# Kernel tuning notes

Measured on AMD Instinct MI355X. Metric: run time of the kernel, lower is better.

The kernel has to match this reference:

```python
import jax, jax.numpy as jnp
import numpy as np
import math

B, L, H, D = 4, 2048, 8, 64
FACTOR = 5
SAMPLE_K = min(FACTOR * int(np.ceil(np.log(L))), L)  # U_part = 40
N_TOP = min(FACTOR * int(np.ceil(np.log(L))), L)     # u = 40


def setup_inputs() -> dict:
    key = jax.random.key(0)
    kq, kk, kv, ki = jax.random.split(key, 4)
    queries = jax.random.normal(kq, (B, L, H, D), dtype=jnp.float32)
    keys = jax.random.normal(kk, (B, L, H, D), dtype=jnp.float32)
    values = jax.random.normal(kv, (B, L, H, D), dtype=jnp.float32)
    # ProbSparse random key sampling indices (torch.randint(L_K, (L_Q, sample_k)))
    index_sample = jax.random.randint(ki, (L, SAMPLE_K), 0, L, dtype=jnp.int64)
    return {"queries": queries, "keys": keys, "values": values,
            "index_sample": index_sample}


def reference(queries, keys, values, index_sample):
    # [B, L, H, D] -> [B, H, L, D]
    Q = jnp.transpose(queries, (0, 2, 1, 3))
    K = jnp.transpose(keys, (0, 2, 1, 3))
    V = jnp.transpose(values, (0, 2, 1, 3))
    L_K = K.shape[2]

    # --- _prob_QK ---
    # gather sampled keys per query: [B, H, L_Q, sample_k, D]
    K_sample = K[:, :, index_sample, :]
    # sampled QK dots: [B, H, L_Q, sample_k]
    Q_K_sample = jnp.einsum('bhld,bhlsd->bhls', Q, K_sample)
    # sparsity measurement M = max - mean
    M = Q_K_sample.max(axis=-1) - Q_K_sample.sum(axis=-1) / L_K  # [B, H, L_Q]
    _, M_top = jax.lax.top_k(M, N_TOP)  # [B, H, n_top]
    # gather top queries: [B, H, n_top, D]
    Q_reduce = jnp.take_along_axis(Q, M_top[..., None], axis=2)
    # reduced scores against all keys: [B, H, n_top, L_K]
    scores_top = jnp.einsum('bhud,bhkd->bhuk', Q_reduce, K)

    # --- forward tail ---
    scale = 1.0 / math.sqrt(D)
    attn = jax.nn.softmax(scores_top * scale, axis=-1)  # dropout = identity (eval)
    context = jnp.einsum('bhuk,bhkd->bhud', attn, V)  # [B, H, n_top, D]
    # [B, n_top, H, D]
    return jnp.transpose(context, (0, 2, 1, 3))
```

## Files before the change

### kernel.cpp

```cpp
#include <hip/hip_runtime.h>
#include <hip/hip_bf16.h>

#define BB 4
#define LL 2048
#define HH 8
#define DD 64
#define SK 40
#define NT 40
#define CH 256
#define NCH (LL / CH)
#define QH 20

#define NPH 5
#define PH 8
#define RS 516
#define PBUF (PH * RS)

typedef __attribute__((address_space(1))) const void* gl_ptr_t;
typedef __attribute__((address_space(3))) void*       lds_ptr_t;

__global__ __launch_bounds__(256) void compute_m_kernel(
        const float* __restrict__ Q, const float* __restrict__ K,
        const int* __restrict__ idx, float* __restrict__ M) {
    __shared__ float kbuf[2 * PBUF];
    __shared__ int sidx[SK];

    int blk = blockIdx.x;
    int x = blk & 7, g = blk >> 3;
    int b = x >> 1;
    int l = (g << 1) | (x & 1);
    int t = threadIdx.x;

    if (t < SK) sidx[t] = idx[(size_t)l * SK + t];

    int q  = t & 3;
    int h  = t >> 5;
    int s0 = (t >> 2) & 7;

    const float4* Qb = (const float4*)(Q + ((size_t)b * LL + l) * 512 + h * 64 + q * 16);
    float4 qf0 = Qb[0], qf1 = Qb[1], qf2 = Qb[2], qf3 = Qb[3];

    const float* Kb = K + (size_t)b * LL * 512;

    int wv   = t >> 6;
    int lane = t & 63;
    __syncthreads();

    #define STAGE(p, buf) do {                                                  \
        _Pragma("unroll")                                                       \
        for (int i = 0; i < 4; ++i) {                                           \
            int r  = wv * 2 + (i >> 1);                                         \
            int hf = i & 1;                                                     \
            const float* gsrc = Kb + (size_t)sidx[(p) * PH + r] * 512           \
                              + hf * 256 + lane * 4;                            \
            float* ldst = kbuf + (buf) * PBUF + r * RS + hf * 256;              \
            __builtin_amdgcn_global_load_lds((gl_ptr_t)gsrc, (lds_ptr_t)ldst,   \
                                             16, 0, 0);                         \
        }                                                                       \
    } while (0)

    STAGE(0, 0);
    __syncthreads();

    float mx = -INFINITY, sm = 0.0f;
    #pragma unroll
    for (int p = 0; p < NPH; ++p) {
        if (p < NPH - 1) STAGE(p + 1, (p + 1) & 1);
        const float* kb = kbuf + (p & 1) * PBUF + s0 * RS + h * 64 + q * 16;
        float4 k0 = *(const float4*)(kb);
        float4 k1 = *(const float4*)(kb + 4);
        float4 k2 = *(const float4*)(kb + 8);
        float4 k3 = *(const float4*)(kb + 12);
        float pd = qf0.x * k0.x + qf0.y * k0.y + qf0.z * k0.z + qf0.w * k0.w
                 + qf1.x * k1.x + qf1.y * k1.y + qf1.z * k1.z + qf1.w * k1.w
                 + qf2.x * k2.x + qf2.y * k2.y + qf2.z * k2.z + qf2.w * k2.w
                 + qf3.x * k3.x + qf3.y * k3.y + qf3.z * k3.z + qf3.w * k3.w;
        pd += __shfl_xor(pd, 1, 64);
        pd += __shfl_xor(pd, 2, 64);
        mx = fmaxf(mx, pd);
        sm += pd;
        if (p < NPH - 1) __syncthreads();
    }
    #undef STAGE

    #pragma unroll
    for (int off = 16; off >= 1; off >>= 1) {
        mx = fmaxf(mx, __shfl_xor(mx, off, 64));
        sm += __shfl_xor(sm, off, 64);
    }
    if ((t & 31) == 0)
        M[((size_t)b * HH + h) * LL + l] = mx - sm * (1.0f / (4.0f * (float)LL));
}

__global__ __launch_bounds__(256) void topk_kernel(const float* __restrict__ M,
                                                   int* __restrict__ topi) {
    __shared__ unsigned long long keys[LL];
    __shared__ unsigned long long wmax[4];
    __shared__ int win;
    int bh = blockIdx.x;
    int t  = threadIdx.x;
    int lane = t & 63, w = t >> 6;

    unsigned long long kmax = 0ULL;
    #pragma unroll
    for (int j = 0; j < 8; ++j) {
        int i = t + 256 * j;
        unsigned int bits = __float_as_uint(M[(size_t)bh * LL + i]);
        bits = (bits & 0x80000000u) ? ~bits : (bits | 0x80000000u);
        unsigned long long k = ((unsigned long long)bits << 11)
                             | (unsigned int)(LL - 1 - i);
        keys[i] = k;
        if (k > kmax) kmax = k;
    }
    __syncthreads();

    for (int u = 0; u < NT; ++u) {
        unsigned long long k = kmax;
        #pragma unroll
        for (int off = 32; off >= 1; off >>= 1) {
            unsigned long long o = __shfl_xor(k, off, 64);
            if (o > k) k = o;
        }
        if (lane == 0) wmax[w] = k;
        __syncthreads();
        if (t == 0) {
            unsigned long long k0 = wmax[0];
            if (wmax[1] > k0) k0 = wmax[1];
            if (wmax[2] > k0) k0 = wmax[2];
            if (wmax[3] > k0) k0 = wmax[3];
            int i = (LL - 1) - (int)(k0 & 0x7FF);
            topi[bh * NT + u] = i;
            keys[i] = 0ULL;
            win = i;
        }
        __syncthreads();
        if ((win & 255) == t) {
            kmax = 0ULL;
            #pragma unroll
            for (int j = 0; j < 8; ++j) {
                unsigned long long kk = keys[t + 256 * j];
                if (kk > kmax) kmax = kk;
            }
        }
    }
}

__global__ __launch_bounds__(256, 3) void attn_kernel(
        const float* __restrict__ Q, const float* __restrict__ K,
        const float* __restrict__ V, const int* __restrict__ topi,
        float2* __restrict__ pml, float* __restrict__ po) {
    __shared__ float  qs[QH][DD];
    __shared__ float4 e4buf[4][64];
    __shared__ float  oarea[4][QH][DD];
    __shared__ float  mlarea[4][QH][2];

    int blk = blockIdx.x;
    int qh  = blk >> 8;
    int cc2 = blk & 255;
    int c   = cc2 & (NCH - 1);
    int bh  = cc2 >> 3;
    int h = bh & (HH - 1), b = bh >> 3;
    int t = threadIdx.x, lane = t & 63, w = t >> 6;
    int u0 = qh * QH;

    for (int i = t; i < QH * DD; i += 256) {
        int u = i >> 6, d = i & 63;
        int lq = topi[bh * NT + u0 + u];
        qs[u][d] = Q[(((size_t)b * LL + lq) * HH + h) * DD + d];
    }

    int key = c * CH + w * 64 + lane;
    const float4* kr = (const float4*)&K[(((size_t)b * LL + key) * HH + h) * DD];
    float4 kreg[16];
    #pragma unroll
    for (int j = 0; j < 16; ++j) kreg[j] = kr[j];

    float vcol[64];
    const float* vb = &V[(((size_t)b * LL + c * CH + w * 64) * HH + h) * DD + lane];
    #pragma unroll
    for (int j = 0; j < 64; ++j) vcol[j] = vb[(size_t)j * HH * DD];

    __syncthreads();

    for (int uq = 0; uq < QH / 4; ++uq) {
        float o0 = 0, o1 = 0, o2 = 0, o3 = 0;
        float mv0, mv1, mv2, mv3, lv0, lv1, lv2, lv3;
        float4 ev;
        #pragma unroll
        for (int j = 0; j < 4; ++j) {
            int u = uq * 4 + j;
            const float4* q4 = (const float4*)&qs[u][0];
            float s = 0.0f;
            #pragma unroll
            for (int cc = 0; cc < 16; ++cc) {
                float4 qv = q4[cc];
                s += qv.x * kreg[cc].x + qv.y * kreg[cc].y
                   + qv.z * kreg[cc].z + qv.w * kreg[cc].w;
            }
            s *= 0.125f;
            float m = s;
            #pragma unroll
            for (int off = 32; off >= 1; off >>= 1)
                m = fmaxf(m, __shfl_xor(m, off, 64));
            float e = __expf(s - m);
            float ls = e;
            #pragma unroll
            for (int off = 32; off >= 1; off >>= 1)
                ls += __shfl_xor(ls, off, 64);
            if (j == 0) { mv0 = m; lv0 = ls; ev.x = e; }
            if (j == 1) { mv1 = m; lv1 = ls; ev.y = e; }
            if (j == 2) { mv2 = m; lv2 = ls; ev.z = e; }
            if (j == 3) { mv3 = m; lv3 = ls; ev.w = e; }
        }
        e4buf[w][lane] = ev;
        asm volatile("s_waitcnt lgkmcnt(0)" ::: "memory");
        #pragma unroll
        for (int l2 = 0; l2 < 64; ++l2) {
            float4 e = e4buf[w][l2];
            float  v = vcol[l2];
            o0 += e.x * v; o1 += e.y * v; o2 += e.z * v; o3 += e.w * v;
        }
        oarea[w][uq * 4 + 0][lane] = o0;
        oarea[w][uq * 4 + 1][lane] = o1;
        oarea[w][uq * 4 + 2][lane] = o2;
        oarea[w][uq * 4 + 3][lane] = o3;
        if (lane == 0) {
            mlarea[w][uq * 4 + 0][0] = mv0; mlarea[w][uq * 4 + 0][1] = lv0;
            mlarea[w][uq * 4 + 1][0] = mv1; mlarea[w][uq * 4 + 1][1] = lv1;
            mlarea[w][uq * 4 + 2][0] = mv2; mlarea[w][uq * 4 + 2][1] = lv2;
            mlarea[w][uq * 4 + 3][0] = mv3; mlarea[w][uq * 4 + 3][1] = lv3;
        }
    }
    __syncthreads();

    for (int i = t; i < QH * DD; i += 256) {
        int u = i >> 6, d = i & 63;
        float m0 = mlarea[0][u][0], m1 = mlarea[1][u][0];
        float m2 = mlarea[2][u][0], m3 = mlarea[3][u][0];
        float mb = fmaxf(fmaxf(m0, m1), fmaxf(m2, m3));
        float s0 = __expf(m0 - mb), s1 = __expf(m1 - mb);
        float s2 = __expf(m2 - mb), s3 = __expf(m3 - mb);
        float ob = oarea[0][u][d] * s0 + oarea[1][u][d] * s1
                 + oarea[2][u][d] * s2 + oarea[3][u][d] * s3;
        int gu = u0 + u;
        po[((size_t)(bh * NT + gu) * NCH + c) * DD + d] = ob;
        if (d == 0) {
            float lb = mlarea[0][u][1] * s0 + mlarea[1][u][1] * s1
                     + mlarea[2][u][1] * s2 + mlarea[3][u][1] * s3;
            pml[(bh * NT + gu) * NCH + c] = make_float2(mb, lb);
        }
    }
}

__global__ __launch_bounds__(256) void merge_kernel(
        const float2* __restrict__ pml, const float* __restrict__ po,
        float* __restrict__ out) {
    int wid  = blockIdx.x * 4 + (threadIdx.x >> 6);
    int lane = threadIdx.x & 63;
    int u  = wid % NT;
    int bh = wid / NT;
    int h = bh & (HH - 1), b = bh >> 3;
    int base = (bh * NT + u) * NCH;

    float m = -INFINITY;
    #pragma unroll
    for (int cc = 0; cc < NCH; ++cc) m = fmaxf(m, pml[base + cc].x);
    float lsum = 0.0f, o = 0.0f;
    #pragma unroll
    for (int cc = 0; cc < NCH; ++cc) {
        float2 ml = pml[base + cc];
        float sc = __expf(ml.x - m);
        lsum += ml.y * sc;
        o    += po[(size_t)(base + cc) * DD + lane] * sc;
    }
    out[(((size_t)b * NT + u) * HH + h) * DD + lane] = o / lsum;
}

extern "C" void kernel_launch(void* const* d_in, const int* in_sizes, int n_in,
                              void* d_out, int out_size, void* d_ws, size_t ws_size,
                              hipStream_t stream) {
    const float* Q   = (const float*)d_in[0];
    const float* K   = (const float*)d_in[1];
    const float* V   = (const float*)d_in[2];
    const int*   idx = (const int*)d_in[3];
    float* out = (float*)d_out;

    char* ws = (char*)d_ws;
    float*  M    = (float*)ws;                        ws += (size_t)BB * HH * LL * sizeof(float);
    int*    topi = (int*)ws;                          ws += (size_t)BB * HH * NT * sizeof(int);
    float2* pml  = (float2*)ws;                       ws += (size_t)BB * HH * NT * NCH * sizeof(float2);
    float*  po   = (float*)ws;

    hipLaunchKernelGGL(compute_m_kernel, dim3(BB * LL), dim3(256), 0, stream,
                       Q, K, idx, M);
    hipLaunchKernelGGL(topk_kernel, dim3(BB * HH), dim3(256), 0, stream, M, topi);
    hipLaunchKernelGGL(attn_kernel, dim3(2 * BB * HH * NCH), dim3(256), 0, stream,
                       Q, K, V, topi, pml, po);
    hipLaunchKernelGGL(merge_kernel, dim3(BB * HH * NT / 4), dim3(256), 0, stream,
                       pml, po, out);
}
```

Baseline: 177.4 us.

## Give each wave private K-sample buffers and drop block barriers in compute_m

The sampled-QK kernel now splits the 40 sampled keys into four slices of ten, one per wave. Each wave loads its keys through registers into its own double-buffered LDS slot, replacing the block-wide async global_load_lds staging and the per-phase __syncthreads with a wave-local lgkmcnt wait. The per-wave max and sum partials are combined through a small shared array, with a single barrier at the end. This removes block-level synchronisation from the loop, at the cost of register-staged copies and a final cross-wave reduction.

```diff
diff --git a/kernel.cpp b/kernel.cpp
--- a/kernel.cpp
+++ b/kernel.cpp
@@ -11,19 +11,15 @@
 #define NCH (LL / CH)
 #define QH 20
 
-#define NPH 5
-#define PH 8
+#define WS 10
 #define RS 516
-#define PBUF (PH * RS)
-
-typedef __attribute__((address_space(1))) const void* gl_ptr_t;
-typedef __attribute__((address_space(3))) void*       lds_ptr_t;
 
 __global__ __launch_bounds__(256) void compute_m_kernel(
         const float* __restrict__ Q, const float* __restrict__ K,
         const int* __restrict__ idx, float* __restrict__ M) {
-    __shared__ float kbuf[2 * PBUF];
+    __shared__ float kbuf[4][2][2 * RS];
     __shared__ int sidx[SK];
+    __shared__ float2 mlpart[4][HH];
 
     int blk = blockIdx.x;
     int x = blk & 7, g = blk >> 3;
@@ -33,40 +29,46 @@
 
     if (t < SK) sidx[t] = idx[(size_t)l * SK + t];
 
-    int q  = t & 3;
-    int h  = t >> 5;
-    int s0 = (t >> 2) & 7;
+    int lane = t & 63, w = t >> 6;
+    int s_lo = lane >> 5;
+    int h    = (lane >> 2) & 7;
+    int q    = lane & 3;
 
     const float4* Qb = (const float4*)(Q + ((size_t)b * LL + l) * 512 + h * 64 + q * 16);
     float4 qf0 = Qb[0], qf1 = Qb[1], qf2 = Qb[2], qf3 = Qb[3];
 
     const float* Kb = K + (size_t)b * LL * 512;
 
-    int wv   = t >> 6;
-    int lane = t & 63;
-    __syncthreads();
-
-    #define STAGE(p, buf) do {                                                  \
-        _Pragma("unroll")                                                       \
-        for (int i = 0; i < 4; ++i) {                                           \
-            int r  = wv * 2 + (i >> 1);                                         \
-            int hf = i & 1;                                                     \
-            const float* gsrc = Kb + (size_t)sidx[(p) * PH + r] * 512           \
-                              + hf * 256 + lane * 4;                            \
-            float* ldst = kbuf + (buf) * PBUF + r * RS + hf * 256;              \
-            __builtin_amdgcn_global_load_lds((gl_ptr_t)gsrc, (lds_ptr_t)ldst,   \
-                                             16, 0, 0);                         \
-        }                                                                       \
+    int r  = lane >> 5;
+    int cw = lane & 31;
+    __syncthreads();
+
+    float4 g0, g1, g2, g3;
+    #define LOADP(p) do {                                                       \
+        const float* src = Kb + (size_t)sidx[w * WS + (p) * 2 + r] * 512        \
+                         + cw * 4;                                              \
+        g0 = *(const float4*)(src);                                             \
+        g1 = *(const float4*)(src + 128);                                       \
+        g2 = *(const float4*)(src + 256);                                       \
+        g3 = *(const float4*)(src + 384);                                       \
     } while (0)
-
-    STAGE(0, 0);
-    __syncthreads();
+    #define WRITEP(slot) do {                                                   \
+        float* dst = &kbuf[w][slot][r * RS + cw * 4];                           \
+        *(float4*)(dst)       = g0;                                             \
+        *(float4*)(dst + 128) = g1;                                             \
+        *(float4*)(dst + 256) = g2;                                             \
+        *(float4*)(dst + 384) = g3;                                             \
+    } while (0)
+
+    LOADP(0);
+    WRITEP(0);
 
     float mx = -INFINITY, sm = 0.0f;
     #pragma unroll
-    for (int p = 0; p < NPH; ++p) {
-        if (p < NPH - 1) STAGE(p + 1, (p + 1) & 1);
-        const float* kb = kbuf + (p & 1) * PBUF + s0 * RS + h * 64 + q * 16;
+    for (int p = 0; p < WS / 2; ++p) {
+        if (p < WS / 2 - 1) LOADP(p + 1);
+        asm volatile("s_waitcnt lgkmcnt(0)" ::: "memory");
+        const float* kb = &kbuf[w][p & 1][s_lo * RS + h * 64 + q * 16];
         float4 k0 = *(const float4*)(kb);
         float4 k1 = *(const float4*)(kb + 4);
         float4 k2 = *(const float4*)(kb + 8);
@@ -79,17 +81,28 @@
         pd += __shfl_xor(pd, 2, 64);
         mx = fmaxf(mx, pd);
         sm += pd;
-        if (p < NPH - 1) __syncthreads();
-    }
-    #undef STAGE
-
-    #pragma unroll
-    for (int off = 16; off >= 1; off >>= 1) {
-        mx = fmaxf(mx, __shfl_xor(mx, off, 64));
-        sm += __shfl_xor(sm, off, 64);
-    }
-    if ((t & 31) == 0)
-        M[((size_t)b * HH + h) * LL + l] = mx - sm * (1.0f / (4.0f * (float)LL));
+        if (p < WS / 2 - 1) WRITEP((p + 1) & 1);
+    }
+    #undef LOADP
+    #undef WRITEP
+
+    mx = fmaxf(mx, __shfl_xor(mx, 32, 64));
+    sm += __shfl_xor(sm, 32, 64);
+
+    if ((lane & 0x23) == 0)
+        mlpart[w][h] = make_float2(mx, sm);
+    __syncthreads();
+
+    if (t < HH) {
+        float MX = -INFINITY, SM = 0.0f;
+        #pragma unroll
+        for (int w2 = 0; w2 < 4; ++w2) {
+            float2 ml = mlpart[w2][t];
+            MX = fmaxf(MX, ml.x);
+            SM += ml.y;
+        }
+        M[((size_t)b * HH + t) * LL + l] = MX - SM * (1.0f / (float)LL);
+    }
 }
 
 __global__ __launch_bounds__(256) void topk_kernel(const float* __restrict__ M,
```

After: 174.1 us. About the same (-1.9%).
